# Kernel tuning notes

Hardware: AMD Instinct MI355X
Metric: run time of the kernel (lower is better)

Reference implementation:

```python
import jax, jax.numpy as jnp
import numpy as np

B, C, L, D, H = 8, 64, 128, 768, 768  # batch, candidates, tokens, hidden, mlp hidden


def setup_inputs() -> dict:
    key = jax.random.key(0)
    k0, k1, k2 = jax.random.split(key, 3)
    inp = jax.random.normal(k0, (B, C, 2, L, D), dtype=jnp.float32)
    # MlpModule params (input_size = 768*2): Linear(2D->H) -> ReLU -> Linear(H->1)
    W1 = jax.random.normal(k1, (2 * D, H), dtype=jnp.float32) * 0.02
    b1 = jnp.zeros((H,), dtype=jnp.float32)
    W2 = jax.random.normal(k2, (H, 1), dtype=jnp.float32) * 0.02
    b2 = jnp.zeros((1,), dtype=jnp.float32)
    return {"input": inp, "W1": W1, "b1": b1, "W2": W2, "b2": b2}


def reference(input, W1, b1, W2, b2):
    b, c, _, l, d = input.shape
    context = input[:, :, 0].reshape(b * c, l, d)  # [BC, L, D]
    entity = input[:, :, 1].reshape(b * c, l, d)   # [BC, L, D]
    mask = (context[:, :, 0] != 0).astype(context.dtype)  # [BC, L]

    # bmm similarity: [BC, L, L]
    sim = jnp.einsum('bld,bmd->blm', context, entity)
    dot_scores = jnp.max(sim, axis=-1)          # [BC, L]
    argmax_values = jnp.argmax(sim, axis=-1)    # [BC, L]

    # gather best-matching entity token per context token: [BC, L, D]
    gathered = jnp.take_along_axis(entity, argmax_values[..., None], axis=1)

    # MLP over stacked (context, entity) pair -> flatten to 2D features
    mlp_in = jnp.concatenate([context, gathered], axis=-1)  # [BC, L, 2D]
    h = jax.nn.relu(mlp_in @ W1 + b1)
    scores = (h @ W2 + b2)[..., 0]              # [BC, L]

    scores = jnp.sum(scores * mask, axis=-1)              # [BC]
    dot_scores = jnp.sum(dot_scores * mask, axis=-1).reshape(b, c)  # [B, C]
    return scores, dot_scores
```

## Files before the change

kernel.cpp:

```cpp
#include <hip/hip_runtime.h>
#include <hip/hip_bf16.h>
#include <stdint.h>

#define NPAIR 512
#define LTOK  128
#define DDIM  768
#define HDIM  768
#define K2    1536
#define MARGIN 0.4f

typedef float f32x4 __attribute__((ext_vector_type(4)));
typedef short bf16x8 __attribute__((ext_vector_type(8)));

static __device__ __forceinline__ unsigned short f2bf(float f) {
    union { float f; uint32_t u; } v; v.f = f;
    uint32_t u = v.u;
    u += 0x7FFF + ((u >> 16) & 1);
    return (unsigned short)(u >> 16);
}

static __device__ __forceinline__ uint2 pack4(f32x4 v) {
    uint2 r;
    r.x = (unsigned)f2bf(v[0]) | ((unsigned)f2bf(v[1]) << 16);
    r.y = (unsigned)f2bf(v[2]) | ((unsigned)f2bf(v[3]) << 16);
    return r;
}

typedef const __attribute__((address_space(1))) void* gas_t;
typedef __attribute__((address_space(3))) void* las_t;
static __device__ __forceinline__ void gld16(const void* g, void* l) {
    __builtin_amdgcn_global_load_lds((gas_t)g, (las_t)l, 16, 0, 0);
}

static __device__ __forceinline__ float wave_dot(const float* __restrict__ a,
                                                 const float* __restrict__ b,
                                                 int lane) {
    f32x4 s4 = {0.f, 0.f, 0.f, 0.f};
#pragma unroll
    for (int it = 0; it < 3; ++it) {
        int k = it * 256 + lane * 4;
        f32x4 av = *(const f32x4*)(a + k);
        f32x4 bv = *(const f32x4*)(b + k);
#pragma unroll
        for (int q = 0; q < 4; ++q) s4[q] = fmaf(av[q], bv[q], s4[q]);
    }
    float v = (s4[0] + s4[1]) + (s4[2] + s4[3]);
#pragma unroll
    for (int m = 1; m < 64; m <<= 1) v += __shfl_xor(v, m);
    return v;
}

__global__ __launch_bounds__(256, 2) void simfma_kernel(
        const float* __restrict__ inp,
        float* __restrict__ dotmax, int* __restrict__ argmax,
        unsigned short* __restrict__ Cbf, unsigned short* __restrict__ Ebf)
{
    const int p    = blockIdx.x;
    const int t    = threadIdx.x;
    const int wv   = t >> 6;
    const int lane = t & 63;
    const int s    = lane & 15, g = lane >> 4;

    const float* Cbase = inp + (size_t)(2 * p) * LTOK * DDIM;
    const float* Ebase = Cbase + (size_t)LTOK * DDIM;

    __shared__ unsigned short Cl[2][128][32];
    __shared__ unsigned short El[2][128][32];
    __shared__ unsigned short cand[128][16];
    __shared__ int   ccnt[128];
    __shared__ float rm1[128];
    __shared__ int   ri1[128];

    if (t < 128) ccnt[t] = 0;

    f32x4 acc[2][8];
#pragma unroll
    for (int i = 0; i < 2; i++)
#pragma unroll
        for (int j = 0; j < 8; j++) acc[i][j] = (f32x4){0.f, 0.f, 0.f, 0.f};

    for (int kc = 0; kc < 12; ++kc) {
        const int k0 = kc * 64;
#pragma unroll
        for (int it = 0; it < 8; ++it) {
            int slot = it * 256 + t;
            int row = slot >> 4, l16 = slot & 15;
            int h = l16 >> 3, kl = (l16 & 7) * 4;
            f32x4 cv = *(const f32x4*)(Cbase + (size_t)row * DDIM + k0 + l16 * 4);
            uint2 cw = pack4(cv);
            *(uint2*)&Cl[h][row][kl] = cw;
            *(uint2*)(Cbf + ((size_t)p * LTOK + row) * DDIM + k0 + l16 * 4) = cw;
        }
#pragma unroll
        for (int it = 0; it < 8; ++it) {
            int slot = it * 256 + t;
            int row = slot >> 4, l16 = slot & 15;
            int h = l16 >> 3, kl = (l16 & 7) * 4;
            f32x4 ev = *(const f32x4*)(Ebase + (size_t)row * DDIM + k0 + l16 * 4);
            uint2 ew = pack4(ev);
            *(uint2*)&El[h][row][kl] = ew;
            *(uint2*)(Ebf + ((size_t)p * LTOK + row) * DDIM + k0 + l16 * 4) = ew;
        }
        __syncthreads();

#pragma unroll
        for (int h = 0; h < 2; ++h) {
            bf16x8 af[2], bfr[8];
#pragma unroll
            for (int i = 0; i < 2; ++i)
                af[i] = *(const bf16x8*)&Cl[h][wv * 32 + i * 16 + s][g * 8];
#pragma unroll
            for (int j = 0; j < 8; ++j)
                bfr[j] = *(const bf16x8*)&El[h][j * 16 + s][g * 8];
#pragma unroll
            for (int i = 0; i < 2; ++i)
#pragma unroll
                for (int j = 0; j < 8; ++j)
                    acc[i][j] = __builtin_amdgcn_mfma_f32_16x16x32_bf16(af[i], bfr[j], acc[i][j], 0, 0, 0);
        }
        __syncthreads();
    }

#pragma unroll
    for (int i = 0; i < 2; ++i)
#pragma unroll
        for (int r = 0; r < 4; ++r) {
            float m1 = acc[i][0][r]; int i1 = s; float m2 = -1e30f;
#pragma unroll
            for (int j = 1; j < 8; ++j) {
                float v = acc[i][j][r]; int c = j * 16 + s;
                if (v > m1 || (v == m1 && c < i1)) { m2 = m1; m1 = v; i1 = c; }
                else if (v > m2) m2 = v;
            }
#pragma unroll
            for (int msk = 1; msk < 16; msk <<= 1) {
                float o1 = __shfl_xor(m1, msk);
                int   oi = __shfl_xor(i1, msk);
                float o2 = __shfl_xor(m2, msk);
                bool take = (o1 > m1) || (o1 == m1 && oi < i1);
                float nm2 = take ? fmaxf(m1, o2) : fmaxf(m2, o1);
                if (take) { m1 = o1; i1 = oi; }
                m2 = nm2;
            }
            int row = wv * 32 + i * 16 + g * 4 + r;
            if (s == 0) { rm1[row] = m1; ri1[row] = i1; }
            float thr = m1 - MARGIN;
#pragma unroll
            for (int j = 0; j < 8; ++j) {
                float v = acc[i][j][r]; int c = j * 16 + s;
                if (v >= thr && c != i1) {
                    int idx = atomicAdd(&ccnt[row], 1);
                    if (idx < 16) cand[row][idx] = (unsigned short)c;
                }
            }
        }
    __syncthreads();

    for (int rr = 0; rr < 32; ++rr) {
        int row = wv + rr * 4;
        int cnt = ccnt[row];
        float m1 = rm1[row]; int i1 = ri1[row];
        size_t ob = (size_t)p * LTOK + row;
        if (cnt == 0) {
            if (lane == 0) { dotmax[ob] = m1; argmax[ob] = i1; }
            continue;
        }
        const float* cr = Cbase + (size_t)row * DDIM;
        float bv; int bc;
        if (cnt <= 16) {
            bv = wave_dot(cr, Ebase + (size_t)i1 * DDIM, lane); bc = i1;
            for (int q = 0; q < cnt; ++q) {
                int c = cand[row][q];
                float v = wave_dot(cr, Ebase + (size_t)c * DDIM, lane);
                if (v > bv || (v == bv && c < bc)) { bv = v; bc = c; }
            }
        } else {
            bv = -1e30f; bc = 0;
            for (int c = 0; c < 128; ++c) {
                float v = wave_dot(cr, Ebase + (size_t)c * DDIM, lane);
                if (v > bv || (v == bv && c < bc)) { bv = v; bc = c; }
            }
        }
        if (lane == 0) { dotmax[ob] = bv; argmax[ob] = bc; }
    }
}

__global__ __launch_bounds__(256) void w1t_kernel(
        const float* __restrict__ W1, unsigned short* __restrict__ W1T)
{
    int idx = blockIdx.x * 256 + threadIdx.x;
    if (idx >= HDIM * K2 / 8) return;
    int c  = idx / (K2 / 8);
    int k0 = (idx % (K2 / 8)) * 8;
    unsigned short v[8];
#pragma unroll
    for (int q = 0; q < 8; q++) v[q] = f2bf(W1[(size_t)(k0 + q) * HDIM + c]);
    *(uint4*)(W1T + (size_t)c * K2 + k0) = *(const uint4*)v;
}

__global__ __launch_bounds__(256, 2) void mlp2_kernel(
        const unsigned short* __restrict__ Cbf,
        const unsigned short* __restrict__ Ebf,
        const unsigned short* __restrict__ W1T,
        const float* __restrict__ b1,
        const float* __restrict__ W2,
        const int* __restrict__ argmax,
        float* __restrict__ tokscore)
{
    const int p    = blockIdx.x;
    const int cbk  = blockIdx.y;
    const int t    = threadIdx.x;
    const int wv   = t >> 6;
    const int lane = t & 63;
    const int s    = lane & 15, g = lane >> 4;
    const int wr   = wv >> 1, wc = wv & 1;

    __shared__ unsigned short Ald[2][128][32];
    __shared__ unsigned short Bld[2][256][32];
    __shared__ int am[128];

    if (t < 128) am[t] = argmax[p * LTOK + t];

    f32x4 acc[4][8];
#pragma unroll
    for (int i = 0; i < 4; i++)
#pragma unroll
        for (int j = 0; j < 8; j++) acc[i][j] = (f32x4){0.f, 0.f, 0.f, 0.f};

    const int rsub = lane >> 2;
    const int chk  = lane & 3;

    for (int kc = 0; kc < 24; ++kc) {
        const int k0   = kc * 64;
        const bool ctx = (kc < 12);
        const int kloc = ctx ? k0 : (k0 - DDIM);

#pragma unroll
        for (int h = 0; h < 2; ++h)
#pragma unroll
            for (int n = 0; n < 4; ++n) {
                int c0  = (wv * 4 + n) * 16;
                int col = c0 + rsub;
                const unsigned short* src =
                    W1T + (size_t)(cbk * 256 + col) * K2 + k0 + h * 32 + chk * 8;
                gld16(src, &Bld[h][c0][0]);
            }
#pragma unroll
        for (int h = 0; h < 2; ++h)
#pragma unroll
            for (int n = 0; n < 2; ++n) {
                int r0 = (wv * 2 + n) * 16;
                int r  = r0 + rsub;
                const unsigned short* base = ctx
                    ? (Cbf + ((size_t)p * LTOK + r) * DDIM)
                    : (Ebf + ((size_t)p * LTOK + am[r]) * DDIM);
                gld16(base + kloc + h * 32 + chk * 8, &Ald[h][r0][0]);
            }
        __syncthreads();

#pragma unroll
        for (int h = 0; h < 2; ++h) {
            bf16x8 af[4], bfr[8];
#pragma unroll
            for (int i = 0; i < 4; ++i)
                af[i] = *(const bf16x8*)&Ald[h][wr * 64 + i * 16 + s][g * 8];
#pragma unroll
            for (int j = 0; j < 8; ++j)
                bfr[j] = *(const bf16x8*)&Bld[h][wc * 128 + j * 16 + s][g * 8];
#pragma unroll
            for (int i = 0; i < 4; ++i)
#pragma unroll
                for (int j = 0; j < 8; ++j)
                    acc[i][j] = __builtin_amdgcn_mfma_f32_16x16x32_bf16(af[i], bfr[j], acc[i][j], 0, 0, 0);
        }
        __syncthreads();
    }

    float w2v[8], b1v[8];
#pragma unroll
    for (int j = 0; j < 8; j++) {
        int col = cbk * 256 + wc * 128 + j * 16 + s;
        w2v[j] = W2[col];
        b1v[j] = b1[col];
    }
    float ssum[4][4];
#pragma unroll
    for (int i = 0; i < 4; i++)
#pragma unroll
        for (int r = 0; r < 4; r++) ssum[i][r] = 0.f;
#pragma unroll
    for (int i = 0; i < 4; i++)
#pragma unroll
        for (int j = 0; j < 8; j++)
#pragma unroll
            for (int r = 0; r < 4; r++) {
                float h = acc[i][j][r] + b1v[j];
                h = h > 0.f ? h : 0.f;
                ssum[i][r] = fmaf(h, w2v[j], ssum[i][r]);
            }
#pragma unroll
    for (int sft = 1; sft < 16; sft <<= 1)
#pragma unroll
        for (int i = 0; i < 4; i++)
#pragma unroll
            for (int r = 0; r < 4; r++) ssum[i][r] += __shfl_xor(ssum[i][r], sft);
    if (s == 0) {
#pragma unroll
        for (int i = 0; i < 4; i++)
#pragma unroll
            for (int r = 0; r < 4; r++)
                atomicAdd(&tokscore[p * LTOK + wr * 64 + i * 16 + g * 4 + r], ssum[i][r]);
    }
}

__global__ __launch_bounds__(256) void sim_fp32_kernel(
        const float* __restrict__ inp,
        float* __restrict__ dotmax, int* __restrict__ argmax)
{
    const int p  = blockIdx.x;
    const int t  = threadIdx.x;
    const int tx = t & 15, ty = t >> 4;
    const float* Cbase = inp + (size_t)(2 * p) * LTOK * DDIM;
    const float* Ebase = Cbase + (size_t)LTOK * DDIM;

    __shared__ float Ct[128][36];
    __shared__ float Et[128][36];

    float acc[8][8];
#pragma unroll
    for (int i = 0; i < 8; i++)
#pragma unroll
        for (int j = 0; j < 8; j++) acc[i][j] = 0.f;

    for (int kc = 0; kc < 24; ++kc) {
        const int k0 = kc * 32;
#pragma unroll
        for (int q = 0; q < 4; ++q) {
            int f = q * 256 + t;
            int row = f >> 3, c4 = f & 7;
            *(f32x4*)&Ct[row][c4 * 4] = *(const f32x4*)(Cbase + (size_t)row * DDIM + k0 + c4 * 4);
            *(f32x4*)&Et[row][c4 * 4] = *(const f32x4*)(Ebase + (size_t)row * DDIM + k0 + c4 * 4);
        }
        __syncthreads();
#pragma unroll
        for (int kk4 = 0; kk4 < 8; ++kk4) {
            f32x4 cr[8], er[8];
#pragma unroll
            for (int i = 0; i < 8; i++) cr[i] = *(const f32x4*)&Ct[ty + 16 * i][kk4 * 4];
#pragma unroll
            for (int j = 0; j < 8; j++) er[j] = *(const f32x4*)&Et[tx + 16 * j][kk4 * 4];
#pragma unroll
            for (int kk = 0; kk < 4; kk++)
#pragma unroll
                for (int i = 0; i < 8; i++)
#pragma unroll
                    for (int j = 0; j < 8; j++)
                        acc[i][j] = fmaf(cr[i][kk], er[j][kk], acc[i][j]);
        }
        __syncthreads();
    }
#pragma unroll
    for (int i = 0; i < 8; i++) {
        float m = acc[i][0]; int mi = tx;
#pragma unroll
        for (int j = 1; j < 8; j++) {
            int c = tx + 16 * j;
            float v = acc[i][j];
            if (v > m || (v == m && c < mi)) { m = v; mi = c; }
        }
#pragma unroll
        for (int sft = 1; sft < 16; sft <<= 1) {
            float vo = __shfl_xor(m, sft);
            int   io = __shfl_xor(mi, sft);
            if (vo > m || (vo == m && io < mi)) { m = vo; mi = io; }
        }
        if (tx == 0) {
            int r = ty + 16 * i;
            dotmax[(size_t)p * LTOK + r] = m;
            argmax[(size_t)p * LTOK + r] = mi;
        }
    }
}

__global__ __launch_bounds__(256, 2) void mlp_kernel(
        const float* __restrict__ inp,
        const unsigned short* __restrict__ W1T,
        const float* __restrict__ b1,
        const float* __restrict__ W2,
        const int* __restrict__ argmax,
        float* __restrict__ tokscore)
{
    const int tile = blockIdx.x;
    const int cb   = blockIdx.y;
    const int t    = threadIdx.x;
    const int wv   = t >> 6;
    const int lane = t & 63;
    const int s    = lane & 15, g = lane >> 4;

    __shared__ unsigned short At[64][32];
    __shared__ unsigned short Bt[384][32];
    __shared__ int am[64];

    if (t < 64) am[t] = argmax[tile * 64 + t];
    __syncthreads();

    f32x4 acc[4][6];
#pragma unroll
    for (int i = 0; i < 4; i++)
#pragma unroll
        for (int j = 0; j < 6; j++) acc[i][j] = (f32x4){0.f, 0.f, 0.f, 0.f};

    for (int kc = 0; kc < 48; ++kc) {
        const int k0  = kc * 32;
        const int sel = (kc >= 24) ? 1 : 0;
        const int kloc = k0 - sel * DDIM;
#pragma unroll
        for (int q = 0; q < 2; ++q) {
            int f = q * 256 + t;
            int row = f >> 3, c4 = f & 7;
            int token = tile * 64 + row;
            int pp = token >> 7;
            int lsel = sel ? am[row] : (token & 127);
            const float* src = inp + ((size_t)(2 * pp + sel) * LTOK + lsel) * DDIM + kloc + c4 * 4;
            f32x4 v = *(const f32x4*)src;
            uint2 pk = pack4(v);
            *(uint2*)&At[row][c4 * 4] = pk;
        }
#pragma unroll
        for (int q = 0; q < 6; ++q) {
            int f = q * 256 + t;
            int colr = f >> 2, q8 = f & 3;
            const unsigned short* src = W1T + (size_t)(cb * 384 + colr) * K2 + k0 + q8 * 8;
            *(uint4*)&Bt[colr][q8 * 8] = *(const uint4*)src;
        }
        __syncthreads();

        bf16x8 af[4], bfr[6];
#pragma unroll
        for (int i = 0; i < 4; i++) af[i]  = *(const bf16x8*)&At[i * 16 + s][g * 8];
#pragma unroll
        for (int j = 0; j < 6; j++) bfr[j] = *(const bf16x8*)&Bt[wv * 96 + j * 16 + s][g * 8];
#pragma unroll
        for (int i = 0; i < 4; i++)
#pragma unroll
            for (int j = 0; j < 6; j++)
                acc[i][j] = __builtin_amdgcn_mfma_f32_16x16x32_bf16(af[i], bfr[j], acc[i][j], 0, 0, 0);
        __syncthreads();
    }

    float w2v[6], b1v[6];
#pragma unroll
    for (int j = 0; j < 6; j++) {
        int col = cb * 384 + wv * 96 + j * 16 + s;
        w2v[j] = W2[col];
        b1v[j] = b1[col];
    }
    float ssum[4][4];
#pragma unroll
    for (int i = 0; i < 4; i++)
#pragma unroll
        for (int r = 0; r < 4; r++) ssum[i][r] = 0.f;
#pragma unroll
    for (int i = 0; i < 4; i++)
#pragma unroll
        for (int j = 0; j < 6; j++)
#pragma unroll
            for (int r = 0; r < 4; r++) {
                float h = acc[i][j][r] + b1v[j];
                h = h > 0.f ? h : 0.f;
                ssum[i][r] = fmaf(h, w2v[j], ssum[i][r]);
            }
#pragma unroll
    for (int sft = 1; sft < 16; sft <<= 1)
#pragma unroll
        for (int i = 0; i < 4; i++)
#pragma unroll
            for (int r = 0; r < 4; r++) ssum[i][r] += __shfl_xor(ssum[i][r], sft);
    if (s == 0) {
#pragma unroll
        for (int i = 0; i < 4; i++)
#pragma unroll
            for (int r = 0; r < 4; r++)
                atomicAdd(&tokscore[tile * 64 + i * 16 + g * 4 + r], ssum[i][r]);
    }
}

__global__ __launch_bounds__(128) void reduce_kernel(
        const float* __restrict__ inp,
        const float* __restrict__ tokscore,
        const float* __restrict__ dotmax,
        const float* __restrict__ b2,
        float* __restrict__ out)
{
    int p = blockIdx.x;
    int l = threadIdx.x;
    float c0  = inp[((size_t)(2 * p) * LTOK + l) * DDIM];
    float msk = (c0 != 0.0f) ? 1.f : 0.f;
    float sc  = (tokscore[p * LTOK + l] + b2[0]) * msk;
    float dm  = dotmax[p * LTOK + l] * msk;
#pragma unroll
    for (int sh = 1; sh < 64; sh <<= 1) {
        sc += __shfl_xor(sc, sh);
        dm += __shfl_xor(dm, sh);
    }
    __shared__ float tmp[4];
    if ((l & 63) == 0) { tmp[(l >> 6) * 2] = sc; tmp[(l >> 6) * 2 + 1] = dm; }
    __syncthreads();
    if (l == 0) {
        out[p]          = tmp[0] + tmp[2];
        out[NPAIR + p]  = tmp[1] + tmp[3];
    }
}

extern "C" void kernel_launch(void* const* d_in, const int* in_sizes, int n_in,
                              void* d_out, int out_size, void* d_ws, size_t ws_size,
                              hipStream_t stream)
{
    const float* inp = (const float*)d_in[0];
    const float* W1  = (const float*)d_in[1];
    const float* b1  = (const float*)d_in[2];
    const float* W2  = (const float*)d_in[3];
    const float* b2  = (const float*)d_in[4];
    float* out = (float*)d_out;

    char* ws = (char*)d_ws;
    unsigned short* W1T   = (unsigned short*)ws;
    float*          dotmx = (float*)(ws + 2359296);
    int*            amax  = (int*)(ws + 2359296 + 262144);
    float*          toksc = (float*)(ws + 2359296 + 2*262144);
    unsigned short* Cbf   = (unsigned short*)(ws + 2359296 + 3*262144);
    unsigned short* Ebf   = Cbf + (size_t)NPAIR * LTOK * DDIM;
    const size_t NEED = 2359296ull + 3ull*262144ull + 2ull*100663296ull;

    const bool big = ws_size >= NEED;

    hipMemsetAsync(toksc, 0, 65536 * sizeof(float), stream);
    w1t_kernel<<<(HDIM * K2 / 8 + 255) / 256, 256, 0, stream>>>(W1, W1T);
    if (big) {
        simfma_kernel<<<NPAIR, 256, 0, stream>>>(inp, dotmx, amax, Cbf, Ebf);
        mlp2_kernel<<<dim3(NPAIR, 3), 256, 0, stream>>>(Cbf, Ebf, W1T, b1, W2, amax, toksc);
    } else {
        sim_fp32_kernel<<<NPAIR, 256, 0, stream>>>(inp, dotmx, amax);
        mlp_kernel<<<dim3(1024, 2), 256, 0, stream>>>(inp, W1T, b1, W2, amax, toksc);
    }
    reduce_kernel<<<NPAIR, 128, 0, stream>>>(inp, toksc, dotmx, b2, out);
}
```

Measured before the change: 324.0 us.

## Double-buffer MLP K-loop and replace atomics with partial-sum reduction

```diff
diff --git a/kernel.cpp b/kernel.cpp
--- a/kernel.cpp
+++ b/kernel.cpp
@@ -20,9 +20,11 @@
 }
 
 static __device__ __forceinline__ uint2 pack4(f32x4 v) {
+    __hip_bfloat162 lo = __float22bfloat162_rn(float2{v[0], v[1]});
+    __hip_bfloat162 hi = __float22bfloat162_rn(float2{v[2], v[3]});
     uint2 r;
-    r.x = (unsigned)f2bf(v[0]) | ((unsigned)f2bf(v[1]) << 16);
-    r.y = (unsigned)f2bf(v[2]) | ((unsigned)f2bf(v[3]) << 16);
+    r.x = *reinterpret_cast<unsigned*>(&lo);
+    r.y = *reinterpret_cast<unsigned*>(&hi);
     return r;
 }
 
@@ -205,7 +207,7 @@
         const float* __restrict__ b1,
         const float* __restrict__ W2,
         const int* __restrict__ argmax,
-        float* __restrict__ tokscore)
+        float* __restrict__ part)
 {
     const int p    = blockIdx.x;
     const int cbk  = blockIdx.y;
@@ -230,50 +232,62 @@
     const int rsub = lane >> 2;
     const int chk  = lane & 3;
 
-    for (int kc = 0; kc < 24; ++kc) {
-        const int k0   = kc * 64;
-        const bool ctx = (kc < 12);
+    auto STAGE = [&](int buf, int kt) {
+        const int k0   = kt * 32;
+        const bool ctx = (kt < 24);
         const int kloc = ctx ? k0 : (k0 - DDIM);
-
-#pragma unroll
-        for (int h = 0; h < 2; ++h)
-#pragma unroll
-            for (int n = 0; n < 4; ++n) {
-                int c0  = (wv * 4 + n) * 16;
-                int col = c0 + rsub;
-                const unsigned short* src =
-                    W1T + (size_t)(cbk * 256 + col) * K2 + k0 + h * 32 + chk * 8;
-                gld16(src, &Bld[h][c0][0]);
-            }
-#pragma unroll
-        for (int h = 0; h < 2; ++h)
-#pragma unroll
-            for (int n = 0; n < 2; ++n) {
-                int r0 = (wv * 2 + n) * 16;
-                int r  = r0 + rsub;
-                const unsigned short* base = ctx
-                    ? (Cbf + ((size_t)p * LTOK + r) * DDIM)
-                    : (Ebf + ((size_t)p * LTOK + am[r]) * DDIM);
-                gld16(base + kloc + h * 32 + chk * 8, &Ald[h][r0][0]);
-            }
-        __syncthreads();
-
-#pragma unroll
-        for (int h = 0; h < 2; ++h) {
-            bf16x8 af[4], bfr[8];
-#pragma unroll
-            for (int i = 0; i < 4; ++i)
-                af[i] = *(const bf16x8*)&Ald[h][wr * 64 + i * 16 + s][g * 8];
+#pragma unroll
+        for (int n = 0; n < 4; ++n) {
+            int c0  = (wv * 4 + n) * 16;
+            int col = c0 + rsub;
+            gld16(W1T + (size_t)(cbk * 256 + col) * K2 + k0 + chk * 8,
+                  &Bld[buf][c0][0]);
+        }
+#pragma unroll
+        for (int n = 0; n < 2; ++n) {
+            int r0 = (wv * 2 + n) * 16;
+            int r  = r0 + rsub;
+            const unsigned short* base = ctx
+                ? (Cbf + ((size_t)p * LTOK + r) * DDIM)
+                : (Ebf + ((size_t)p * LTOK + am[r]) * DDIM);
+            gld16(base + kloc + chk * 8, &Ald[buf][r0][0]);
+        }
+    };
+
+    STAGE(0, 0);
+    __syncthreads();
+
+    int cur = 0;
+    for (int kt = 0; kt < 47; ++kt) {
+        STAGE(cur ^ 1, kt + 1);
+        bf16x8 af[4], bfr[8];
+#pragma unroll
+        for (int i = 0; i < 4; ++i)
+            af[i] = *(const bf16x8*)&Ald[cur][wr * 64 + i * 16 + s][g * 8];
+#pragma unroll
+        for (int j = 0; j < 8; ++j)
+            bfr[j] = *(const bf16x8*)&Bld[cur][wc * 128 + j * 16 + s][g * 8];
+#pragma unroll
+        for (int i = 0; i < 4; ++i)
 #pragma unroll
             for (int j = 0; j < 8; ++j)
-                bfr[j] = *(const bf16x8*)&Bld[h][wc * 128 + j * 16 + s][g * 8];
-#pragma unroll
-            for (int i = 0; i < 4; ++i)
-#pragma unroll
-                for (int j = 0; j < 8; ++j)
-                    acc[i][j] = __builtin_amdgcn_mfma_f32_16x16x32_bf16(af[i], bfr[j], acc[i][j], 0, 0, 0);
-        }
-        __syncthreads();
+                acc[i][j] = __builtin_amdgcn_mfma_f32_16x16x32_bf16(af[i], bfr[j], acc[i][j], 0, 0, 0);
+        __syncthreads();
+        cur ^= 1;
+    }
+    {
+        bf16x8 af[4], bfr[8];
+#pragma unroll
+        for (int i = 0; i < 4; ++i)
+            af[i] = *(const bf16x8*)&Ald[cur][wr * 64 + i * 16 + s][g * 8];
+#pragma unroll
+        for (int j = 0; j < 8; ++j)
+            bfr[j] = *(const bf16x8*)&Bld[cur][wc * 128 + j * 16 + s][g * 8];
+#pragma unroll
+        for (int i = 0; i < 4; ++i)
+#pragma unroll
+            for (int j = 0; j < 8; ++j)
+                acc[i][j] = __builtin_amdgcn_mfma_f32_16x16x32_bf16(af[i], bfr[j], acc[i][j], 0, 0, 0);
     }
 
     float w2v[8], b1v[8];
@@ -305,11 +319,44 @@
 #pragma unroll
             for (int r = 0; r < 4; r++) ssum[i][r] += __shfl_xor(ssum[i][r], sft);
     if (s == 0) {
+        const int q = cbk * 2 + wc;
 #pragma unroll
         for (int i = 0; i < 4; i++)
 #pragma unroll
             for (int r = 0; r < 4; r++)
-                atomicAdd(&tokscore[p * LTOK + wr * 64 + i * 16 + g * 4 + r], ssum[i][r]);
+                part[(size_t)q * (NPAIR * LTOK) + p * LTOK + wr * 64 + i * 16 + g * 4 + r]
+                    = ssum[i][r];
+    }
+}
+
+__global__ __launch_bounds__(128) void reduce6_kernel(
+        const float* __restrict__ inp,
+        const float* __restrict__ part,
+        const float* __restrict__ dotmax,
+        const float* __restrict__ b2,
+        float* __restrict__ out)
+{
+    int p = blockIdx.x;
+    int l = threadIdx.x;
+    float c0  = inp[((size_t)(2 * p) * LTOK + l) * DDIM];
+    float msk = (c0 != 0.0f) ? 1.f : 0.f;
+    float sc = b2[0];
+#pragma unroll
+    for (int q = 0; q < 6; ++q)
+        sc += part[(size_t)q * (NPAIR * LTOK) + p * LTOK + l];
+    sc *= msk;
+    float dm = dotmax[p * LTOK + l] * msk;
+#pragma unroll
+    for (int sh = 1; sh < 64; sh <<= 1) {
+        sc += __shfl_xor(sc, sh);
+        dm += __shfl_xor(dm, sh);
+    }
+    __shared__ float tmp[4];
+    if ((l & 63) == 0) { tmp[(l >> 6) * 2] = sc; tmp[(l >> 6) * 2 + 1] = dm; }
+    __syncthreads();
+    if (l == 0) {
+        out[p]          = tmp[0] + tmp[2];
+        out[NPAIR + p]  = tmp[1] + tmp[3];
     }
 }
 
@@ -530,18 +577,20 @@
     float*          toksc = (float*)(ws + 2359296 + 2*262144);
     unsigned short* Cbf   = (unsigned short*)(ws + 2359296 + 3*262144);
     unsigned short* Ebf   = Cbf + (size_t)NPAIR * LTOK * DDIM;
-    const size_t NEED = 2359296ull + 3ull*262144ull + 2ull*100663296ull;
+    float*          part  = (float*)(ws + 2359296 + 3*262144 + 2*100663296ull);
+    const size_t NEED = 2359296ull + 3ull*262144ull + 2ull*100663296ull + 6ull*262144ull;
 
     const bool big = ws_size >= NEED;
 
-    hipMemsetAsync(toksc, 0, 65536 * sizeof(float), stream);
     w1t_kernel<<<(HDIM * K2 / 8 + 255) / 256, 256, 0, stream>>>(W1, W1T);
     if (big) {
         simfma_kernel<<<NPAIR, 256, 0, stream>>>(inp, dotmx, amax, Cbf, Ebf);
-        mlp2_kernel<<<dim3(NPAIR, 3), 256, 0, stream>>>(Cbf, Ebf, W1T, b1, W2, amax, toksc);
+        mlp2_kernel<<<dim3(NPAIR, 3), 256, 0, stream>>>(Cbf, Ebf, W1T, b1, W2, amax, part);
+        reduce6_kernel<<<NPAIR, 128, 0, stream>>>(inp, part, dotmx, b2, out);
     } else {
+        hipMemsetAsync(toksc, 0, 65536 * sizeof(float), stream);
         sim_fp32_kernel<<<NPAIR, 256, 0, stream>>>(inp, dotmx, amax);
         mlp_kernel<<<dim3(1024, 2), 256, 0, stream>>>(inp, W1T, b1, W2, amax, toksc);
-    }
-    reduce_kernel<<<NPAIR, 128, 0, stream>>>(inp, toksc, dotmx, b2, out);
-}
+        reduce_kernel<<<NPAIR, 128, 0, stream>>>(inp, toksc, dotmx, b2, out);
+    }
+}
```

Measured after the change: 328.9 us. About the same (+1.5%).
